# Performance work log

Hardware: AMD Instinct MI355X
Metric: run time of the kernel (lower is better)

## Reference

```python
import jax, jax.numpy as jnp
import numpy as np

P0 = 2   # tublet_size
P = 16   # patch_size
FC = 2   # flow channels (map_x, map_y)


def patchify(x, p0, p1, p2):
    # x: (B, C, T, H, W) -> (B, (T/p0)(H/p1)(W/p2), p0*p1*p2*C)
    B, C, T, H, W = x.shape
    x = x.reshape(B, C, T // p0, p0, H // p1, p1, W // p2, p2)
    x = x.transpose(0, 2, 4, 6, 3, 5, 7, 1)  # b t h w p0 p1 p2 c
    return x.reshape(B, (T // p0) * (H // p1) * (W // p2), p0 * p1 * p2 * C)


def unpatchify(x, p0, p1, p2, C, T, H, W):
    # x: (B, N, p0*p1*p2*C) -> (B, C, T, H, W)
    B = x.shape[0]
    x = x.reshape(B, T // p0, H // p1, W // p2, p0, p1, p2, C)
    x = x.transpose(0, 7, 1, 4, 2, 5, 3, 6)  # b c t p0 h p1 w p2
    return x.reshape(B, C, T, H, W)


def bilinear_warp(imgs, mx, my):
    # imgs: (B, C, T, H, W); mx, my: (B, T, H, W) absolute sample coords.
    # Equivalent of cv2.remap INTER_LINEAR with constant (zero) border.
    B, C, T, H, W = imgs.shape
    x0 = jnp.floor(mx)
    y0 = jnp.floor(my)
    wx = (mx - x0).reshape(B, 1, T, H * W)
    wy = (my - y0).reshape(B, 1, T, H * W)
    x0i = x0.astype(jnp.int32)
    y0i = y0.astype(jnp.int32)
    imgs_flat = imgs.reshape(B, C, T, H * W)

    def gather(yi, xi):
        yc = jnp.clip(yi, 0, H - 1)
        xc = jnp.clip(xi, 0, W - 1)
        idx = (yc * W + xc).reshape(B, 1, T, H * W)
        v = jnp.take_along_axis(imgs_flat, jnp.broadcast_to(idx, (B, C, T, H * W)), axis=-1)
        valid = ((yi >= 0) & (yi <= H - 1) & (xi >= 0) & (xi <= W - 1)).reshape(B, 1, T, H * W)
        return v * valid.astype(v.dtype)

    v00 = gather(y0i, x0i)
    v01 = gather(y0i, x0i + 1)
    v10 = gather(y0i + 1, x0i)
    v11 = gather(y0i + 1, x0i + 1)
    out = (v00 * (1 - wx) * (1 - wy) + v01 * wx * (1 - wy)
           + v10 * (1 - wx) * wy + v11 * wx * wy)
    return out.reshape(B, C, T, H, W)


def setup_inputs() -> dict:
    key = jax.random.key(0)
    k1, k2, k3 = jax.random.split(key, 3)
    B, C, T, H, W = 8, 3, 16, 224, 224
    N = (T // P0) * (H // P) * (W // P)         # 1568 tokens
    D = P0 * P * P * FC                         # 1024 per-token flow dim
    output = jax.random.normal(k1, (B, N, D), dtype=jnp.float32)
    raw_target = jax.random.normal(k2, (B, C, T, H, W), dtype=jnp.float32)
    mask = jax.random.randint(k3, (B, N), 0, 2) > 0
    return {"output": output, "raw_target": raw_target, "mask": mask}


def reference(output, raw_target, mask):
    B, C, T, H, W = raw_target.shape
    # tokens -> dense flow field (B, 2, T, H, W)
    flows = unpatchify(output, P0, P, P, FC, T, H, W)
    gx = jnp.arange(W, dtype=flows.dtype)               # (W,)
    gy = jnp.arange(H, dtype=flows.dtype)[:, None]      # (H, 1)
    mx = flows[:, 0] + gx                                # (B, T, H, W)
    my = flows[:, 1] + gy
    recons = bilinear_warp(raw_target, mx, my)           # (B, C, T, H, W)
    rec_p = patchify(recons, P0, P, P)                   # (B, N, p0*p1*p2*C)
    tgt_p = patchify(raw_target, P0, P, P)
    m = mask.astype(rec_p.dtype)[..., None]              # (B, N, 1)
    diff2 = (rec_p - tgt_p) ** 2 * m
    denom = jnp.maximum(m.sum(), 1.0) * rec_p.shape[-1]
    return diff2.sum() / denom
```

## Files before the change

kernel.cpp:

```cpp
#include <hip/hip_runtime.h>

#define Bd 8
#define Cd 3
#define Td 16
#define Hd 224
#define Wd 224
#define Nd 1568
#define Dd 1024
#define HWd (Hd*Wd)
#define MASK_N (Bd*Nd)
#define PATCH_ELEMS 1536.0

#define WIN 24
#define PITCH 24
#define PLANE (WIN*PITCH)
#define BUF (6*PLANE)
#define GRID_MAIN 1024
#define STG_V4 864

struct TokGeo { int b, t2, ph, pw, WX, WY; };

__device__ __forceinline__ TokGeo geo(int tk) {
    TokGeo g;
    g.b = tk / Nd;
    int n = tk - g.b * Nd;
    g.t2 = n / 196;
    int rem = n - g.t2 * 196;
    g.ph = rem / 14;
    g.pw = rem - g.ph * 14;
    g.WX = min(max(g.pw * 16 - 4, 0), Wd - WIN);
    g.WY = min(max(g.ph * 16 - 4, 0), Hd - WIN);
    return g;
}

__device__ __forceinline__ void stg_geom(int j, int& ldsoff, int& goff) {
    int p   = j / 144;
    int rem = j - p * 144;
    int r   = rem / 6;
    int c4  = (rem - r * 6) << 2;
    ldsoff = p * PLANE + r * PITCH + c4;
    goff   = (p >> 1) * (16 * HWd) + (p & 1) * HWd + r * Wd + c4;
}

__device__ __forceinline__ float compute_tok(const float* __restrict__ raw,
                                             const float* __restrict__ pl0,
                                             const TokGeo& g, int tid,
                                             float2 f0, float2 f1) {
    const int i1 = tid >> 4, i2 = tid & 15;
    const int h = (g.ph << 4) + i1;
    const int w = (g.pw << 4) + i2;
    const int tIdx = (h - g.WY) * PITCH + (w - g.WX);
    float acc = 0.f;
    #pragma unroll
    for (int i0 = 0; i0 < 2; ++i0) {
        float2 f = i0 ? f1 : f0;
        float mx = f.x + (float)w;
        float my = f.y + (float)h;

        float x0 = floorf(mx), y0 = floorf(my);
        float wx = mx - x0,    wy = my - y0;
        int x0i = (int)x0, y0i = (int)y0;
        int x1i = x0i + 1, y1i = y0i + 1;

        bool vx0 = (x0i >= 0) && (x0i < Wd);
        bool vx1 = (x1i >= 0) && (x1i < Wd);
        bool vy0 = (y0i >= 0) && (y0i < Hd);
        bool vy1 = (y1i >= 0) && (y1i < Hd);

        int xc0 = min(max(x0i, 0), Wd - 1);
        int xc1 = min(max(x1i, 0), Wd - 1);
        int yc0 = min(max(y0i, 0), Hd - 1);
        int yc1 = min(max(y1i, 0), Hd - 1);

        float w00 = (1.f - wx) * (1.f - wy) * ((vx0 && vy0) ? 1.f : 0.f);
        float w01 = wx         * (1.f - wy) * ((vx1 && vy0) ? 1.f : 0.f);
        float w10 = (1.f - wx) * wy         * ((vx0 && vy1) ? 1.f : 0.f);
        float w11 = wx         * wy         * ((vx1 && vy1) ? 1.f : 0.f);

        const int lx0 = xc0 - g.WX, lx1 = xc1 - g.WX;
        const int ly0 = yc0 - g.WY, ly1 = yc1 - g.WY;
        const bool ok = (lx0 >= 0) & (lx1 < WIN) & (ly0 >= 0) & (ly1 < WIN);

        if (ok) {
            const int b00 = ly0 * PITCH + lx0;
            const int b01 = ly0 * PITCH + lx1;
            const int b10 = ly1 * PITCH + lx0;
            const int b11 = ly1 * PITCH + lx1;
            #pragma unroll
            for (int c = 0; c < Cd; ++c) {
                const float* pl = pl0 + ((c << 1) | i0) * PLANE;
                float rec = pl[b00] * w00 + pl[b01] * w01
                          + pl[b10] * w10 + pl[b11] * w11;
                float d = rec - pl[tIdx];
                acc += d * d;
            }
        } else {
            const int i00 = yc0 * Wd + xc0;
            const int i01 = yc0 * Wd + xc1;
            const int i10 = yc1 * Wd + xc0;
            const int i11 = yc1 * Wd + xc1;
            const float* base = raw + ((size_t)g.b * 48 + (size_t)g.t2 * 2 + i0) * HWd;
            #pragma unroll
            for (int c = 0; c < Cd; ++c) {
                const float* img = base + c * (16 * HWd);
                float rec = img[i00] * w00 + img[i01] * w01
                          + img[i10] * w10 + img[i11] * w11;
                const float* pl = pl0 + ((c << 1) | i0) * PLANE;
                float d = rec - pl[tIdx];
                acc += d * d;
            }
        }
    }
    return acc;
}

__global__ void compact_kernel(const int* __restrict__ mask,
                               int* __restrict__ list,
                               unsigned int* __restrict__ cnt) {
    int i = blockIdx.x * 256 + threadIdx.x;
    bool m = (i < MASK_N) && (mask[i] != 0);
    unsigned long long bal = __ballot(m);
    int lane = threadIdx.x & 63;
    int wid  = threadIdx.x >> 6;
    unsigned pre  = (unsigned)__popcll(bal & ((1ull << lane) - 1ull));
    unsigned wtot = (unsigned)__popcll(bal);
    __shared__ unsigned wt[4];
    __shared__ unsigned bbase;
    if (lane == 0) wt[wid] = wtot;
    __syncthreads();
    if (threadIdx.x == 0)
        bbase = atomicAdd(cnt, wt[0] + wt[1] + wt[2] + wt[3]);
    __syncthreads();
    unsigned base = bbase;
    for (int k = 0; k < wid; ++k) base += wt[k];
    if (m) list[base + pre] = i;
}

__global__ __launch_bounds__(256, 4)
void flow_mse_main(const float* __restrict__ outp,
                   const float* __restrict__ raw,
                   const int* __restrict__ list,
                   const unsigned int* __restrict__ cntp,
                   float* __restrict__ partial) {
    __shared__ float lds[2 * BUF];
    __shared__ float sdata[4];
    const int tid = threadIdx.x;
    const int cnt = (int)*cntp;

    int l0, l1, l2, l3, q0, q1, q2, q3;
    stg_geom(tid,       l0, q0);
    stg_geom(tid + 256, l1, q1);
    stg_geom(tid + 512, l2, q2);
    const bool k3 = tid < (STG_V4 - 768);
    stg_geom(k3 ? tid + 768 : 0, l3, q3);

    float4 s0, s1, s2, s3;
    float2 fc0, fc1, fn0, fn1;
    TokGeo gc, gn;
    float acc = 0.f;

    int idx = blockIdx.x;
    int cur = 0;

    if (idx < cnt) {
        int tk = list[idx];
        gc = geo(tk);
        const float* base = raw + ((size_t)gc.b * 48 + (size_t)gc.t2 * 2) * HWd
                          + gc.WY * Wd + gc.WX;
        s0 = *(const float4*)(base + q0);
        s1 = *(const float4*)(base + q1);
        s2 = *(const float4*)(base + q2);
        if (k3) s3 = *(const float4*)(base + q3);
        const float2* fp = (const float2*)(outp + (size_t)tk * Dd);
        fc0 = fp[tid]; fc1 = fp[256 + tid];
        *(float4*)(lds + l0) = s0;
        *(float4*)(lds + l1) = s1;
        *(float4*)(lds + l2) = s2;
        if (k3) *(float4*)(lds + l3) = s3;
    }

    while (idx < cnt) {
        int nidx = idx + GRID_MAIN;
        __syncthreads();
        bool have_next = nidx < cnt;
        if (have_next) {
            int ntk = list[nidx];
            gn = geo(ntk);
            const float* base = raw + ((size_t)gn.b * 48 + (size_t)gn.t2 * 2) * HWd
                              + gn.WY * Wd + gn.WX;
            s0 = *(const float4*)(base + q0);
            s1 = *(const float4*)(base + q1);
            s2 = *(const float4*)(base + q2);
            if (k3) s3 = *(const float4*)(base + q3);
            const float2* fp = (const float2*)(outp + (size_t)ntk * Dd);
            fn0 = fp[tid]; fn1 = fp[256 + tid];
        }
        acc += compute_tok(raw, lds + cur * BUF, gc, tid, fc0, fc1);
        if (have_next) {
            float* dst = lds + (cur ^ 1) * BUF;
            *(float4*)(dst + l0) = s0;
            *(float4*)(dst + l1) = s1;
            *(float4*)(dst + l2) = s2;
            if (k3) *(float4*)(dst + l3) = s3;
        }
        idx = nidx; cur ^= 1;
        gc = gn; fc0 = fn0; fc1 = fn1;
    }

    for (int off = 32; off > 0; off >>= 1) acc += __shfl_down(acc, off, 64);
    if ((tid & 63) == 0) sdata[tid >> 6] = acc;
    __syncthreads();
    if (tid == 0)
        partial[blockIdx.x] = sdata[0] + sdata[1] + sdata[2] + sdata[3];
}

__global__ void finalize_kernel(const float* __restrict__ partial,
                                const int* __restrict__ mask,
                                float* __restrict__ out) {
    double s = 0.0;
    for (int i = threadIdx.x; i < GRID_MAIN; i += blockDim.x)
        s += (double)partial[i];
    int cnt = 0;
    for (int i = threadIdx.x; i < MASK_N; i += blockDim.x)
        cnt += (mask[i] != 0) ? 1 : 0;
    for (int off = 32; off > 0; off >>= 1) {
        s   += __shfl_down(s, off, 64);
        cnt += __shfl_down(cnt, off, 64);
    }
    __shared__ double sdat[4];
    __shared__ int    cdat[4];
    int lane = threadIdx.x & 63, wid = threadIdx.x >> 6;
    if (lane == 0) { sdat[wid] = s; cdat[wid] = cnt; }
    __syncthreads();
    if (threadIdx.x == 0) {
        double st = sdat[0] + sdat[1] + sdat[2] + sdat[3];
        int ct = cdat[0] + cdat[1] + cdat[2] + cdat[3];
        double denom = (double)(ct > 0 ? ct : 1) * PATCH_ELEMS;
        out[0] = (float)(st / denom);
    }
}

extern "C" void kernel_launch(void* const* d_in, const int* in_sizes, int n_in,
                              void* d_out, int out_size, void* d_ws, size_t ws_size,
                              hipStream_t stream) {
    const float* outp = (const float*)d_in[0];
    const float* raw  = (const float*)d_in[1];
    const int*   mask = (const int*)d_in[2];
    float* out = (float*)d_out;

    unsigned int* cnt = (unsigned int*)d_ws;
    float* partial = (float*)((char*)d_ws + 16);
    int*   list    = (int*)((char*)d_ws + 16 + GRID_MAIN * 4);

    hipMemsetAsync(d_ws, 0, 16, stream);

    compact_kernel<<<(MASK_N + 255) / 256, 256, 0, stream>>>(mask, list, cnt);
    flow_mse_main<<<GRID_MAIN, 256, 0, stream>>>(outp, raw, list, cnt, partial);
    finalize_kernel<<<1, 256, 0, stream>>>(partial, mask, out);
}
```

Before: 170.0 us.

## Shrink staged window to patch, single-block compaction, reuse count in finalize

The LDS staging window shrinks from a 24x24 halo tile to the exact 16x16 patch. Samples that fall outside the patch now take the global-memory fallback path, which cuts staging traffic and LDS use so occupancy (launch bounds 6) and the grid size (2048) can rise. Mask compaction becomes a single 1024-thread block that writes the count directly, which removes the memset and the atomics, and finalize reuses that count instead of rescanning the mask. The trade-off is that more bilinear taps go to global memory when the flow moves samples off the patch, and the compaction is now serial.

```diff
diff --git a/kernel.cpp b/kernel.cpp
--- a/kernel.cpp
+++ b/kernel.cpp
@@ -11,14 +11,13 @@
 #define MASK_N (Bd*Nd)
 #define PATCH_ELEMS 1536.0
 
-#define WIN 24
-#define PITCH 24
-#define PLANE (WIN*PITCH)
+#define WINP 16
+#define PLANE 256
 #define BUF (6*PLANE)
-#define GRID_MAIN 1024
-#define STG_V4 864
-
-struct TokGeo { int b, t2, ph, pw, WX, WY; };
+#define GRID_MAIN 2048
+#define STG_V4 384
+
+struct TokGeo { int b, t2, ph, pw; };
 
 __device__ __forceinline__ TokGeo geo(int tk) {
     TokGeo g;
@@ -28,28 +27,24 @@
     int rem = n - g.t2 * 196;
     g.ph = rem / 14;
     g.pw = rem - g.ph * 14;
-    g.WX = min(max(g.pw * 16 - 4, 0), Wd - WIN);
-    g.WY = min(max(g.ph * 16 - 4, 0), Hd - WIN);
     return g;
 }
 
-__device__ __forceinline__ void stg_geom(int j, int& ldsoff, int& goff) {
-    int p   = j / 144;
-    int rem = j - p * 144;
-    int r   = rem / 6;
-    int c4  = (rem - r * 6) << 2;
-    ldsoff = p * PLANE + r * PITCH + c4;
-    goff   = (p >> 1) * (16 * HWd) + (p & 1) * HWd + r * Wd + c4;
+__device__ __forceinline__ int stg_goff(int j) {
+    int p   = j >> 6;
+    int rem = j & 63;
+    int r   = rem >> 2;
+    int c4  = (rem & 3) << 2;
+    return (p >> 1) * (16 * HWd) + (p & 1) * HWd + r * Wd + c4;
 }
 
 __device__ __forceinline__ float compute_tok(const float* __restrict__ raw,
                                              const float* __restrict__ pl0,
                                              const TokGeo& g, int tid,
                                              float2 f0, float2 f1) {
-    const int i1 = tid >> 4, i2 = tid & 15;
-    const int h = (g.ph << 4) + i1;
-    const int w = (g.pw << 4) + i2;
-    const int tIdx = (h - g.WY) * PITCH + (w - g.WX);
+    const int WX = g.pw << 4, WY = g.ph << 4;
+    const int h = WY + (tid >> 4);
+    const int w = WX + (tid & 15);
     float acc = 0.f;
     #pragma unroll
     for (int i0 = 0; i0 < 2; ++i0) {
@@ -77,21 +72,21 @@
         float w10 = (1.f - wx) * wy         * ((vx0 && vy1) ? 1.f : 0.f);
         float w11 = wx         * wy         * ((vx1 && vy1) ? 1.f : 0.f);
 
-        const int lx0 = xc0 - g.WX, lx1 = xc1 - g.WX;
-        const int ly0 = yc0 - g.WY, ly1 = yc1 - g.WY;
-        const bool ok = (lx0 >= 0) & (lx1 < WIN) & (ly0 >= 0) & (ly1 < WIN);
+        const int lx0 = xc0 - WX, lx1 = xc1 - WX;
+        const int ly0 = yc0 - WY, ly1 = yc1 - WY;
+        const bool ok = (lx0 >= 0) & (lx1 < WINP) & (ly0 >= 0) & (ly1 < WINP);
 
         if (ok) {
-            const int b00 = ly0 * PITCH + lx0;
-            const int b01 = ly0 * PITCH + lx1;
-            const int b10 = ly1 * PITCH + lx0;
-            const int b11 = ly1 * PITCH + lx1;
+            const int b00 = (ly0 << 4) + lx0;
+            const int b01 = (ly0 << 4) + lx1;
+            const int b10 = (ly1 << 4) + lx0;
+            const int b11 = (ly1 << 4) + lx1;
             #pragma unroll
             for (int c = 0; c < Cd; ++c) {
                 const float* pl = pl0 + ((c << 1) | i0) * PLANE;
                 float rec = pl[b00] * w00 + pl[b01] * w01
                           + pl[b10] * w10 + pl[b11] * w11;
-                float d = rec - pl[tIdx];
+                float d = rec - pl[tid & 255];
                 acc += d * d;
             }
         } else {
@@ -99,14 +94,14 @@
             const int i01 = yc0 * Wd + xc1;
             const int i10 = yc1 * Wd + xc0;
             const int i11 = yc1 * Wd + xc1;
-            const float* base = raw + ((size_t)g.b * 48 + (size_t)g.t2 * 2 + i0) * HWd;
+            const float* base = raw + (size_t)(g.b * 48 + (g.t2 << 1) + i0) * HWd;
             #pragma unroll
             for (int c = 0; c < Cd; ++c) {
                 const float* img = base + c * (16 * HWd);
                 float rec = img[i00] * w00 + img[i01] * w01
                           + img[i10] * w10 + img[i11] * w11;
                 const float* pl = pl0 + ((c << 1) | i0) * PLANE;
-                float d = rec - pl[tIdx];
+                float d = rec - pl[tid & 255];
                 acc += d * d;
             }
         }
@@ -117,26 +112,31 @@
 __global__ void compact_kernel(const int* __restrict__ mask,
                                int* __restrict__ list,
                                unsigned int* __restrict__ cnt) {
-    int i = blockIdx.x * 256 + threadIdx.x;
-    bool m = (i < MASK_N) && (mask[i] != 0);
-    unsigned long long bal = __ballot(m);
-    int lane = threadIdx.x & 63;
-    int wid  = threadIdx.x >> 6;
-    unsigned pre  = (unsigned)__popcll(bal & ((1ull << lane) - 1ull));
-    unsigned wtot = (unsigned)__popcll(bal);
-    __shared__ unsigned wt[4];
-    __shared__ unsigned bbase;
-    if (lane == 0) wt[wid] = wtot;
-    __syncthreads();
-    if (threadIdx.x == 0)
-        bbase = atomicAdd(cnt, wt[0] + wt[1] + wt[2] + wt[3]);
-    __syncthreads();
-    unsigned base = bbase;
-    for (int k = 0; k < wid; ++k) base += wt[k];
-    if (m) list[base + pre] = i;
-}
-
-__global__ __launch_bounds__(256, 4)
+    const int tid = threadIdx.x;
+    __shared__ unsigned wt[16];
+    unsigned base = 0;
+    for (int i0 = 0; i0 < MASK_N; i0 += 1024) {
+        int i = i0 + tid;
+        bool m = (i < MASK_N) && (mask[i] != 0);
+        unsigned long long bal = __ballot(m);
+        int lane = tid & 63, wid = tid >> 6;
+        unsigned pre  = (unsigned)__popcll(bal & ((1ull << lane) - 1ull));
+        unsigned wtot = (unsigned)__popcll(bal);
+        if (lane == 0) wt[wid] = wtot;
+        __syncthreads();
+        unsigned wbase = base;
+        for (int k = 0; k < wid; ++k) wbase += wt[k];
+        if (m) list[wbase + pre] = i;
+        unsigned tot = 0;
+        #pragma unroll
+        for (int k = 0; k < 16; ++k) tot += wt[k];
+        base += tot;
+        __syncthreads();
+    }
+    if (tid == 0) *cnt = base;
+}
+
+__global__ __launch_bounds__(256, 6)
 void flow_mse_main(const float* __restrict__ outp,
                    const float* __restrict__ raw,
                    const int* __restrict__ list,
@@ -147,14 +147,13 @@
     const int tid = threadIdx.x;
     const int cnt = (int)*cntp;
 
-    int l0, l1, l2, l3, q0, q1, q2, q3;
-    stg_geom(tid,       l0, q0);
-    stg_geom(tid + 256, l1, q1);
-    stg_geom(tid + 512, l2, q2);
-    const bool k3 = tid < (STG_V4 - 768);
-    stg_geom(k3 ? tid + 768 : 0, l3, q3);
-
-    float4 s0, s1, s2, s3;
+    const int q0 = stg_goff(tid);
+    const bool k1 = tid < (STG_V4 - 256);
+    const int q1 = stg_goff(k1 ? tid + 256 : 0);
+    const int l0 = tid << 2;
+    const int l1 = (tid << 2) + 1024;
+
+    float4 s0, s1;
     float2 fc0, fc1, fn0, fn1;
     TokGeo gc, gn;
     float acc = 0.f;
@@ -165,18 +164,14 @@
     if (idx < cnt) {
         int tk = list[idx];
         gc = geo(tk);
-        const float* base = raw + ((size_t)gc.b * 48 + (size_t)gc.t2 * 2) * HWd
-                          + gc.WY * Wd + gc.WX;
+        const float* base = raw + (size_t)(gc.b * 48 + (gc.t2 << 1)) * HWd
+                          + (gc.ph << 4) * Wd + (gc.pw << 4);
         s0 = *(const float4*)(base + q0);
-        s1 = *(const float4*)(base + q1);
-        s2 = *(const float4*)(base + q2);
-        if (k3) s3 = *(const float4*)(base + q3);
-        const float2* fp = (const float2*)(outp + (size_t)tk * Dd);
+        if (k1) s1 = *(const float4*)(base + q1);
+        const float2* fp = (const float2*)(outp + ((size_t)tk << 10));
         fc0 = fp[tid]; fc1 = fp[256 + tid];
         *(float4*)(lds + l0) = s0;
-        *(float4*)(lds + l1) = s1;
-        *(float4*)(lds + l2) = s2;
-        if (k3) *(float4*)(lds + l3) = s3;
+        if (k1) *(float4*)(lds + l1) = s1;
     }
 
     while (idx < cnt) {
@@ -186,22 +181,18 @@
         if (have_next) {
             int ntk = list[nidx];
             gn = geo(ntk);
-            const float* base = raw + ((size_t)gn.b * 48 + (size_t)gn.t2 * 2) * HWd
-                              + gn.WY * Wd + gn.WX;
+            const float* base = raw + (size_t)(gn.b * 48 + (gn.t2 << 1)) * HWd
+                              + (gn.ph << 4) * Wd + (gn.pw << 4);
             s0 = *(const float4*)(base + q0);
-            s1 = *(const float4*)(base + q1);
-            s2 = *(const float4*)(base + q2);
-            if (k3) s3 = *(const float4*)(base + q3);
-            const float2* fp = (const float2*)(outp + (size_t)ntk * Dd);
+            if (k1) s1 = *(const float4*)(base + q1);
+            const float2* fp = (const float2*)(outp + ((size_t)ntk << 10));
             fn0 = fp[tid]; fn1 = fp[256 + tid];
         }
         acc += compute_tok(raw, lds + cur * BUF, gc, tid, fc0, fc1);
         if (have_next) {
             float* dst = lds + (cur ^ 1) * BUF;
             *(float4*)(dst + l0) = s0;
-            *(float4*)(dst + l1) = s1;
-            *(float4*)(dst + l2) = s2;
-            if (k3) *(float4*)(dst + l3) = s3;
+            if (k1) *(float4*)(dst + l1) = s1;
         }
         idx = nidx; cur ^= 1;
         gc = gn; fc0 = fn0; fc1 = fn1;
@@ -215,27 +206,21 @@
 }
 
 __global__ void finalize_kernel(const float* __restrict__ partial,
-                                const int* __restrict__ mask,
+                                const unsigned int* __restrict__ cntp,
                                 float* __restrict__ out) {
     double s = 0.0;
     for (int i = threadIdx.x; i < GRID_MAIN; i += blockDim.x)
         s += (double)partial[i];
-    int cnt = 0;
-    for (int i = threadIdx.x; i < MASK_N; i += blockDim.x)
-        cnt += (mask[i] != 0) ? 1 : 0;
-    for (int off = 32; off > 0; off >>= 1) {
-        s   += __shfl_down(s, off, 64);
-        cnt += __shfl_down(cnt, off, 64);
-    }
+    for (int off = 32; off > 0; off >>= 1)
+        s += __shfl_down(s, off, 64);
     __shared__ double sdat[4];
-    __shared__ int    cdat[4];
     int lane = threadIdx.x & 63, wid = threadIdx.x >> 6;
-    if (lane == 0) { sdat[wid] = s; cdat[wid] = cnt; }
+    if (lane == 0) sdat[wid] = s;
     __syncthreads();
     if (threadIdx.x == 0) {
         double st = sdat[0] + sdat[1] + sdat[2] + sdat[3];
-        int ct = cdat[0] + cdat[1] + cdat[2] + cdat[3];
-        double denom = (double)(ct > 0 ? ct : 1) * PATCH_ELEMS;
+        unsigned ct = *cntp;
+        double denom = (double)(ct > 0u ? ct : 1u) * PATCH_ELEMS;
         out[0] = (float)(st / denom);
     }
 }
@@ -252,9 +237,7 @@
     float* partial = (float*)((char*)d_ws + 16);
     int*   list    = (int*)((char*)d_ws + 16 + GRID_MAIN * 4);
 
-    hipMemsetAsync(d_ws, 0, 16, stream);
-
-    compact_kernel<<<(MASK_N + 255) / 256, 256, 0, stream>>>(mask, list, cnt);
+    compact_kernel<<<1, 1024, 0, stream>>>(mask, list, cnt);
     flow_mse_main<<<GRID_MAIN, 256, 0, stream>>>(outp, raw, list, cnt, partial);
-    finalize_kernel<<<1, 256, 0, stream>>>(partial, mask, out);
-}
+    finalize_kernel<<<1, 256, 0, stream>>>(partial, cnt, out);
+}
```

Measured after the change: 171.2 us. No clear change (+0.7%).
